# Kernel tuning notes

Hardware: AMD Instinct MI355X
Metric: run time of the kernel (lower is better)

Reference implementation:

```python
import jax, jax.numpy as jnp
import numpy as np

B, N, D = 64, 100, 32            # batch, nodes, node feature size
FE = [96, 160, 192]              # edge-MLP layer sizes
FN = [256, 256, 32]              # node-MLP layer sizes
ALPHA = 0.2                      # leaky relu slope


def _lin_init(key, fan_in, fan_out):
    kw, kb = jax.random.split(key)
    bound = 1.0 / np.sqrt(fan_in)
    w = jax.random.uniform(kw, (fan_in, fan_out), jnp.float32, -bound, bound)
    b = jax.random.uniform(kb, (fan_out,), jnp.float32, -bound, bound)
    return w, b


def setup_inputs() -> dict:
    key = jax.random.key(0)
    ks = jax.random.split(key, 7)
    d = {"x": jax.random.normal(ks[0], (B, N, D), jnp.float32)}
    fe_sizes = [2 * D] + FE                    # edge MLP: in = concat(x_i, x_j)
    fn_sizes = [FE[-1] + D] + FN               # node MLP: in = concat(agg, x)
    for li in range(3):
        w, b = _lin_init(ks[1 + li], fe_sizes[li], fe_sizes[li + 1])
        d[f"fe_w{li}"], d[f"fe_b{li}"] = w, b
    for li in range(3):
        w, b = _lin_init(ks[4 + li], fn_sizes[li], fn_sizes[li + 1])
        d[f"fn_w{li}"], d[f"fn_b{li}"] = w, b
    return d


def reference(x, fe_w0, fe_b0, fe_w1, fe_b1, fe_w2, fe_b2,
              fn_w0, fn_b0, fn_w1, fn_b1, fn_w2, fn_b2):
    b, n, d = x.shape
    lr = lambda v: jax.nn.leaky_relu(v, ALPHA)
    # fully-connected pairwise edge features: A[b,i,j] = concat(x_i, x_j)
    xi = jnp.broadcast_to(x[:, :, None, :], (b, n, n, d))
    xj = jnp.broadcast_to(x[:, None, :, :], (b, n, n, d))
    a = jnp.concatenate([xi, xj], axis=-1)          # [b, n, n, 2d]
    # edge MLP (fe): leaky relu after every layer (final_linear=False)
    a = lr(a @ fe_w0 + fe_b0)
    a = lr(a @ fe_w1 + fe_b1)
    a = lr(a @ fe_w2 + fe_b2)                       # [b, n, n, FE[-1]]
    # sum aggregation over neighbors j
    agg = jnp.sum(a, axis=2)                        # [b, n, FE[-1]]
    # node MLP (fn): final layer linear (final_linear=True)
    h = jnp.concatenate([agg, x], axis=-1)          # [b, n, FE[-1]+d]
    h = lr(h @ fn_w0 + fn_b0)
    h = lr(h @ fn_w1 + fn_b1)
    h = h @ fn_w2 + fn_b2                           # [b, n, FN[-1]]
    return h
```

## Files before the change

### kernel.cpp

```cpp
#include <hip/hip_runtime.h>

#define B_    64
#define N_    100
#define D_    32
#define F0    96
#define F1    160
#define F2    192
#define HID   256
#define FOUT  32

typedef unsigned short u16;
typedef unsigned int   u32;
typedef u16   u16x8 __attribute__((ext_vector_type(8)));
typedef u32   u32x2 __attribute__((ext_vector_type(2)));
typedef __bf16 bf16x8 __attribute__((ext_vector_type(8)));
typedef float  fx4   __attribute__((ext_vector_type(4)));

__device__ __forceinline__ u16 f2bf(float f) {
    return __builtin_bit_cast(u16, (__bf16)f);
}
__device__ __forceinline__ float lrelu(float v) { return fmaxf(v, 0.2f * v); }

__device__ __forceinline__ bf16x8 fragLds(const u16* p) {
    return __builtin_bit_cast(bf16x8, *(const u16x8*)p);
}
__device__ __forceinline__ bf16x8 fragGbl(const u16* __restrict__ p) {
    return __builtin_bit_cast(bf16x8, *(const u16x8*)p);
}
#define MFMA(a, b, c) __builtin_amdgcn_mfma_f32_16x16x32_bf16((a), (b), (c), 0, 0, 0)

__device__ __forceinline__ u32x2 quadPack(u32 h) {
    u32 h1 = (u32)__shfl_xor((int)h, 1, 64);
    u32 pk = h | (h1 << 16);
    u32 pko = (u32)__shfl_xor((int)pk, 2, 64);
    return (u32x2){pk, pko};
}

#define OFF_P     0u
#define OFF_V     2457600u
#define OFF_AGG   4915200u
#define OFF_PACK  7372800u
#define PK_W1     0
#define PK_W2     15360
#define PK_N0     46080
#define PK_N1     103424
#define PK_N2     168960
#define PK_TOTAL  177152

#define PV_BLOCKS 1200
#define PACK_BLOCKS 346

__global__ __launch_bounds__(512) void prep_kernel(
    const float* __restrict__ x,
    const float* __restrict__ few0,
    const float* __restrict__ few1, const float* __restrict__ few2,
    const float* __restrict__ fnw0, const float* __restrict__ fnw1,
    const float* __restrict__ fnw2,
    float* __restrict__ V, u16* __restrict__ wpack)
{
    const int blk = blockIdx.x, tid = threadIdx.x;
    if (blk < PV_BLOCKS) {
        int o = blk * 512 + tid;
        int r = o / F0, k = o - r * F0;
        const float* xr = x + r * D_;
        float acc = 0.f;
        #pragma unroll
        for (int d = 0; d < D_; ++d) acc = fmaf(xr[d], few0[(D_ + d) * F0 + k], acc);
        V[r * F0 + k] = acc;
    } else {
        int p = (blk - PV_BLOCKS) * 512 + tid;
        const float* src; int start, Ncols, NT;
        if (p < PK_W2)      { start = PK_W1; src = few1; Ncols = F1;   NT = 10; }
        else if (p < PK_N0) { start = PK_W2; src = few2; Ncols = F2;   NT = 12; }
        else if (p < PK_N1) { start = PK_N0; src = fnw0; Ncols = HID;  NT = 16; }
        else if (p < PK_N2) { start = PK_N1; src = fnw1; Ncols = HID;  NT = 16; }
        else                { start = PK_N2; src = fnw2; Ncols = FOUT; NT = 2;  }
        int local = p - start;
        int j = local & 7, lane = (local >> 3) & 63, rest = local >> 9;
        int nt = rest % NT, kt = rest / NT;
        int n = 16 * nt + (lane & 15);
        int k = 32 * kt + 8 * (lane >> 4) + j;
        wpack[p] = f2bf(src[k * Ncols + n]);
    }
}

__global__ __launch_bounds__(512, 4) void edge_kernel(
    const float* __restrict__ x, const float* __restrict__ few0,
    const float* __restrict__ feb0, const float* __restrict__ V,
    const u16* __restrict__ W1p, const u16* __restrict__ W2p,
    const float* __restrict__ feb1, const float* __restrict__ feb2,
    u16* __restrict__ agg)
{
    const int i = blockIdx.x, b = blockIdx.y;
    const int tid = threadIdx.x, ld = tid & 63, wv = tid >> 6;
    const int wn = wv & 3, wm = wv >> 2;
    const int row = b * N_ + i;

    __shared__ __align__(16) u16  sA0p[7 * 3 * 512];
    __shared__ __align__(16) u16  sA1p[7 * 5 * 512];
    __shared__ __align__(16) float sP[F0];
    __shared__ __align__(16) float sAggP[2 * F2];

    if (tid < F0) {
        const float* xr = x + (size_t)row * D_;
        float acc = feb0[tid];
        #pragma unroll
        for (int d = 0; d < D_; ++d) acc = fmaf(xr[d], few0[d * F0 + tid], acc);
        sP[tid] = acc;
    }
    __syncthreads();

    {
        const float* Vb = V + (size_t)b * N_ * F0;
        #pragma unroll
        for (int s = 0; s < 3; ++s) {
            int idx = tid + 512 * s;
            if (idx < 1344) {
                int lane = idx & 63, rest = idx >> 6;
                int kt = rest % 3, mt = rest / 3;
                int k = 32 * kt + 8 * (lane >> 4);
                int m = 16 * mt + (lane & 15);
                u16x8 w;
                if (m < N_) {
                    const float* vp = Vb + m * F0 + k;
                    fx4 v0 = *(const fx4*)(vp);
                    fx4 v1 = *(const fx4*)(vp + 4);
                    fx4 p0 = *(const fx4*)(sP + k);
                    fx4 p1 = *(const fx4*)(sP + k + 4);
                    #pragma unroll
                    for (int jj = 0; jj < 4; ++jj) {
                        w[jj]     = f2bf(lrelu(p0[jj] + v0[jj]));
                        w[4 + jj] = f2bf(lrelu(p1[jj] + v1[jj]));
                    }
                } else {
                    w = (u16x8){0, 0, 0, 0, 0, 0, 0, 0};
                }
                *(u16x8*)(sA0p + idx * 8) = w;
            }
        }
    }
    __syncthreads();

    const int mtB = wm ? 4 : 0, mtE = wm ? 7 : 4;
    const int c = ld & 15, rlo = (ld >> 4) * 4;
    const int a1off = (ld * 16) ^ (((ld >> 3) & 7) << 4);

    {
        const int nCnt = (wn < 2) ? 3 : 2;
        bf16x8 bw[3][3]; float bias[3];
        #pragma unroll
        for (int t = 0; t < 3; ++t) if (t < nCnt) {
            int nt = wn + 4 * t;
            bias[t] = feb1[16 * nt + c];
            #pragma unroll
            for (int kt = 0; kt < 3; ++kt)
                bw[t][kt] = fragGbl(W1p + (size_t)((kt * 10 + nt) * 64 + ld) * 8);
        }
        for (int mt = mtB; mt < mtE; ++mt) {
            bf16x8 a[3];
            #pragma unroll
            for (int kt = 0; kt < 3; ++kt)
                a[kt] = fragLds(sA0p + ((mt * 3 + kt) * 64 + ld) * 8);
            fx4 acc[3];
            #pragma unroll
            for (int t = 0; t < 3; ++t) acc[t] = (fx4){0.f, 0.f, 0.f, 0.f};
            #pragma unroll
            for (int kt = 0; kt < 3; ++kt)
                #pragma unroll
                for (int t = 0; t < 3; ++t)
                    if (t < nCnt) acc[t] = MFMA(a[kt], bw[t][kt], acc[t]);
            #pragma unroll
            for (int t = 0; t < 3; ++t) if (t < nCnt) {
                int nt = wn + 4 * t;
                int f = 16 * nt + c;
                int lq = (f >> 3) & 3;
                int S  = (((rlo >> 3) + 2 * lq) & 7) << 4;
                char* base = (char*)sA1p + (mt * 5 + (nt >> 1)) * 1024 + (c & 4) * 2;
                #pragma unroll
                for (int r = 0; r < 4; ++r) {
                    u32 h = (u32)f2bf(lrelu(acc[t][r] + bias[t]));
                    u32x2 two = quadPack(h);
                    int rowl = rlo + 16 * lq + r;
                    if ((ld & 3) == 0)
                        *(u32x2*)(base + ((rowl * 16) ^ S)) = two;
                }
            }
        }
    }
    __syncthreads();

    {
        bf16x8 bw[3][5]; float bias[3];
        float aggp[3] = {0.f, 0.f, 0.f};
        #pragma unroll
        for (int t = 0; t < 3; ++t) {
            int nt = wn + 4 * t;
            bias[t] = feb2[16 * nt + c];
            #pragma unroll
            for (int kt = 0; kt < 5; ++kt)
                bw[t][kt] = fragGbl(W2p + (size_t)((kt * 12 + nt) * 64 + ld) * 8);
        }
        for (int mt = mtB; mt < mtE; ++mt) {
            bf16x8 a[5];
            const char* rb = (const char*)sA1p + mt * 5120 + a1off;
            #pragma unroll
            for (int kt = 0; kt < 5; ++kt)
                a[kt] = fragLds((const u16*)(rb + kt * 1024));
            fx4 acc[3];
            #pragma unroll
            for (int t = 0; t < 3; ++t) acc[t] = (fx4){0.f, 0.f, 0.f, 0.f};
            #pragma unroll
            for (int kt = 0; kt < 5; ++kt)
                #pragma unroll
                for (int t = 0; t < 3; ++t)
                    acc[t] = MFMA(a[kt], bw[t][kt], acc[t]);
            bool ok = (mt < 6) || (rlo == 0);
            if (ok) {
                #pragma unroll
                for (int t = 0; t < 3; ++t)
                    #pragma unroll
                    for (int r = 0; r < 4; ++r)
                        aggp[t] += lrelu(acc[t][r] + bias[t]);
            }
        }
        #pragma unroll
        for (int t = 0; t < 3; ++t) {
            aggp[t] += __shfl_xor(aggp[t], 16, 64);
            aggp[t] += __shfl_xor(aggp[t], 32, 64);
        }
        if (ld < 16) {
            #pragma unroll
            for (int t = 0; t < 3; ++t)
                sAggP[wm * F2 + 16 * (wn + 4 * t) + ld] = aggp[t];
        }
    }
    __syncthreads();

    if (tid < F2) {
        float v = sAggP[tid] + sAggP[F2 + tid];
        agg[(size_t)row * F2 + tid] = f2bf(v);
    }
}

__global__ __launch_bounds__(512, 4) void node_kernel(
    const u16* __restrict__ agg, const float* __restrict__ x,
    const u16* __restrict__ n0p, const u16* __restrict__ n1p,
    const u16* __restrict__ n2p,
    const float* __restrict__ fnb0, const float* __restrict__ fnb1,
    const float* __restrict__ fnb2,
    float* __restrict__ out)
{
    const int blk = blockIdx.x;
    const int tid = threadIdx.x, ld = tid & 63, wv = tid >> 6;
    const int c = ld & 15, rlo = (ld >> 4) * 4;
    const int c0 = c & ~3;

    __shared__ __align__(16) u16 sH0p[7 * 512];
    __shared__ __align__(16) u16 sH1p[8 * 512];
    __shared__ __align__(16) u16 sH2p[8 * 512];

    if (tid < 448) {
        int lane = tid & 63, kt = tid >> 6;
        int k = 32 * kt + 8 * (lane >> 4);
        int m = lane & 15;
        int g = 16 * blk + m;
        u16x8 w;
        if (k < F2) {
            w = *(const u16x8*)(agg + (size_t)g * F2 + k);
        } else {
            const float* xp = x + (size_t)g * D_ + (k - F2);
            fx4 v0 = *(const fx4*)xp;
            fx4 v1 = *(const fx4*)(xp + 4);
            #pragma unroll
            for (int jj = 0; jj < 4; ++jj) {
                w[jj] = f2bf(v0[jj]); w[4 + jj] = f2bf(v1[jj]);
            }
        }
        *(u16x8*)(sH0p + tid * 8) = w;
    }
    __syncthreads();

    {
        fx4 acc[2];
        #pragma unroll
        for (int t = 0; t < 2; ++t) acc[t] = (fx4){0.f, 0.f, 0.f, 0.f};
        for (int kt = 0; kt < 7; ++kt) {
            bf16x8 a = fragLds(sH0p + (kt * 64 + ld) * 8);
            #pragma unroll
            for (int t = 0; t < 2; ++t) {
                int nt = wv + 8 * t;
                bf16x8 bw = fragGbl(n0p + (size_t)((kt * 16 + nt) * 64 + ld) * 8);
                acc[t] = MFMA(a, bw, acc[t]);
            }
        }
        #pragma unroll
        for (int t = 0; t < 2; ++t) {
            int f = 16 * (wv + 8 * t) + c;
            float bias = fnb0[f];
            int kt2 = f >> 5, lq = (f >> 3) & 3;
            u16* basep = sH1p + (kt2 * 64 + rlo + 16 * lq) * 8 + (c0 & 7);
            #pragma unroll
            for (int r = 0; r < 4; ++r) {
                u32 h = (u32)f2bf(lrelu(acc[t][r] + bias));
                u32x2 two = quadPack(h);
                if ((ld & 3) == 0)
                    *(u32x2*)(basep + r * 8) = two;
            }
        }
    }
    __syncthreads();

    {
        fx4 acc[2];
        #pragma unroll
        for (int t = 0; t < 2; ++t) acc[t] = (fx4){0.f, 0.f, 0.f, 0.f};
        for (int kt = 0; kt < 8; ++kt) {
            bf16x8 a = fragLds(sH1p + (kt * 64 + ld) * 8);
            #pragma unroll
            for (int t = 0; t < 2; ++t) {
                int nt = wv + 8 * t;
                bf16x8 bw = fragGbl(n1p + (size_t)((kt * 16 + nt) * 64 + ld) * 8);
                acc[t] = MFMA(a, bw, acc[t]);
            }
        }
        #pragma unroll
        for (int t = 0; t < 2; ++t) {
            int f = 16 * (wv + 8 * t) + c;
            float bias = fnb1[f];
            int kt2 = f >> 5, lq = (f >> 3) & 3;
            u16* basep = sH2p + (kt2 * 64 + rlo + 16 * lq) * 8 + (c0 & 7);
            #pragma unroll
            for (int r = 0; r < 4; ++r) {
                u32 h = (u32)f2bf(lrelu(acc[t][r] + bias));
                u32x2 two = quadPack(h);
                if ((ld & 3) == 0)
                    *(u32x2*)(basep + r * 8) = two;
            }
        }
    }
    __syncthreads();

    if (wv < 2) {
        int nt = wv;
        fx4 acc = (fx4){0.f, 0.f, 0.f, 0.f};
        for (int kt = 0; kt < 8; ++kt) {
            bf16x8 a = fragLds(sH2p + (kt * 64 + ld) * 8);
            bf16x8 bw = fragGbl(n2p + (size_t)((kt * 2 + nt) * 64 + ld) * 8);
            acc = MFMA(a, bw, acc);
        }
        int f = 16 * nt + c;
        float bias = fnb2[f];
        #pragma unroll
        for (int r = 0; r < 4; ++r) {
            int g = 16 * blk + rlo + r;
            out[(size_t)g * FOUT + f] = acc[r] + bias;
        }
    }
}

extern "C" void kernel_launch(void* const* d_in, const int* in_sizes, int n_in,
                              void* d_out, int out_size, void* d_ws, size_t ws_size,
                              hipStream_t stream) {
    const float* x    = (const float*)d_in[0];
    const float* few0 = (const float*)d_in[1];
    const float* feb0 = (const float*)d_in[2];
    const float* few1 = (const float*)d_in[3];
    const float* feb1 = (const float*)d_in[4];
    const float* few2 = (const float*)d_in[5];
    const float* feb2 = (const float*)d_in[6];
    const float* fnw0 = (const float*)d_in[7];
    const float* fnb0 = (const float*)d_in[8];
    const float* fnw1 = (const float*)d_in[9];
    const float* fnb1 = (const float*)d_in[10];
    const float* fnw2 = (const float*)d_in[11];
    const float* fnb2 = (const float*)d_in[12];

    char* w = (char*)d_ws;
    float* V    = (float*)(w + OFF_V);
    u16*   aggb = (u16*)(w + OFF_AGG);
    u16*   pack = (u16*)(w + OFF_PACK);

    prep_kernel<<<PV_BLOCKS + PACK_BLOCKS, 512, 0, stream>>>(
        x, few0, few1, few2, fnw0, fnw1, fnw2, V, pack);

    edge_kernel<<<dim3(N_, B_), 512, 0, stream>>>(
        x, few0, feb0, V, pack + PK_W1, pack + PK_W2, feb1, feb2, aggb);

    node_kernel<<<400, 512, 0, stream>>>(
        aggb, x, pack + PK_N0, pack + PK_N1, pack + PK_N2,
        fnb0, fnb1, fnb2, (float*)d_out);
}
```

Before: 239.1 us.

## Assign one M-tile per wave in edge MLP, fusing layers without barrier

```diff
diff --git a/kernel.cpp b/kernel.cpp
--- a/kernel.cpp
+++ b/kernel.cpp
@@ -93,13 +93,12 @@
 {
     const int i = blockIdx.x, b = blockIdx.y;
     const int tid = threadIdx.x, ld = tid & 63, wv = tid >> 6;
-    const int wn = wv & 3, wm = wv >> 2;
     const int row = b * N_ + i;
 
     __shared__ __align__(16) u16  sA0p[7 * 3 * 512];
     __shared__ __align__(16) u16  sA1p[7 * 5 * 512];
     __shared__ __align__(16) float sP[F0];
-    __shared__ __align__(16) float sAggP[2 * F2];
+    __shared__ __align__(16) float sAggP[7 * F2];
 
     if (tid < F0) {
         const float* xr = x + (size_t)row * D_;
@@ -141,37 +140,39 @@
     }
     __syncthreads();
 
-    const int mtB = wm ? 4 : 0, mtE = wm ? 7 : 4;
     const int c = ld & 15, rlo = (ld >> 4) * 4;
     const int a1off = (ld * 16) ^ (((ld >> 3) & 7) << 4);
 
-    {
-        const int nCnt = (wn < 2) ? 3 : 2;
-        bf16x8 bw[3][3]; float bias[3];
-        #pragma unroll
-        for (int t = 0; t < 3; ++t) if (t < nCnt) {
-            int nt = wn + 4 * t;
-            bias[t] = feb1[16 * nt + c];
+    if (wv < 7) {
+        const int mt = wv;
+
+        bf16x8 a0[3];
+        #pragma unroll
+        for (int kt = 0; kt < 3; ++kt)
+            a0[kt] = fragLds(sA0p + ((mt * 3 + kt) * 64 + ld) * 8);
+        #pragma unroll
+        for (int g = 0; g < 4; ++g) {
+            const int cnt = (g < 3) ? 3 : 1;
+            bf16x8 bw[3][3]; float bias[3];
+            #pragma unroll
+            for (int t = 0; t < 3; ++t) if (t < cnt) {
+                int nt = 3 * g + t;
+                bias[t] = feb1[16 * nt + c];
+                #pragma unroll
+                for (int kt = 0; kt < 3; ++kt)
+                    bw[t][kt] = fragGbl(W1p + (size_t)((kt * 10 + nt) * 64 + ld) * 8);
+            }
+            fx4 acc[3];
+            #pragma unroll
+            for (int t = 0; t < 3; ++t) acc[t] = (fx4){0.f, 0.f, 0.f, 0.f};
             #pragma unroll
             for (int kt = 0; kt < 3; ++kt)
-                bw[t][kt] = fragGbl(W1p + (size_t)((kt * 10 + nt) * 64 + ld) * 8);
-        }
-        for (int mt = mtB; mt < mtE; ++mt) {
-            bf16x8 a[3];
-            #pragma unroll
-            for (int kt = 0; kt < 3; ++kt)
-                a[kt] = fragLds(sA0p + ((mt * 3 + kt) * 64 + ld) * 8);
-            fx4 acc[3];
-            #pragma unroll
-            for (int t = 0; t < 3; ++t) acc[t] = (fx4){0.f, 0.f, 0.f, 0.f};
-            #pragma unroll
-            for (int kt = 0; kt < 3; ++kt)
                 #pragma unroll
                 for (int t = 0; t < 3; ++t)
-                    if (t < nCnt) acc[t] = MFMA(a[kt], bw[t][kt], acc[t]);
-            #pragma unroll
-            for (int t = 0; t < 3; ++t) if (t < nCnt) {
-                int nt = wn + 4 * t;
+                    if (t < cnt) acc[t] = MFMA(a0[kt], bw[t][kt], acc[t]);
+            #pragma unroll
+            for (int t = 0; t < 3; ++t) if (t < cnt) {
+                int nt = 3 * g + t;
                 int f = 16 * nt + c;
                 int lq = (f >> 3) & 3;
                 int S  = (((rlo >> 3) + 2 * lq) & 7) << 4;
@@ -186,58 +187,59 @@
                 }
             }
         }
-    }
-    __syncthreads();
-
-    {
-        bf16x8 bw[3][5]; float bias[3];
-        float aggp[3] = {0.f, 0.f, 0.f};
-        #pragma unroll
-        for (int t = 0; t < 3; ++t) {
-            int nt = wn + 4 * t;
-            bias[t] = feb2[16 * nt + c];
+
+        bf16x8 a1[5];
+        {
+            const char* rb = (const char*)sA1p + mt * 5120 + a1off;
             #pragma unroll
             for (int kt = 0; kt < 5; ++kt)
-                bw[t][kt] = fragGbl(W2p + (size_t)((kt * 12 + nt) * 64 + ld) * 8);
-        }
-        for (int mt = mtB; mt < mtE; ++mt) {
-            bf16x8 a[5];
-            const char* rb = (const char*)sA1p + mt * 5120 + a1off;
+                a1[kt] = fragLds((const u16*)(rb + kt * 1024));
+        }
+        #pragma unroll
+        for (int g = 0; g < 4; ++g) {
+            bf16x8 bw[3][5]; float bias[3];
+            #pragma unroll
+            for (int t = 0; t < 3; ++t) {
+                int nt = 3 * g + t;
+                bias[t] = feb2[16 * nt + c];
+                #pragma unroll
+                for (int kt = 0; kt < 5; ++kt)
+                    bw[t][kt] = fragGbl(W2p + (size_t)((kt * 12 + nt) * 64 + ld) * 8);
+            }
+            fx4 acc[3];
+            #pragma unroll
+            for (int t = 0; t < 3; ++t) acc[t] = (fx4){0.f, 0.f, 0.f, 0.f};
             #pragma unroll
             for (int kt = 0; kt < 5; ++kt)
-                a[kt] = fragLds((const u16*)(rb + kt * 1024));
-            fx4 acc[3];
-            #pragma unroll
-            for (int t = 0; t < 3; ++t) acc[t] = (fx4){0.f, 0.f, 0.f, 0.f};
-            #pragma unroll
-            for (int kt = 0; kt < 5; ++kt)
                 #pragma unroll
                 for (int t = 0; t < 3; ++t)
-                    acc[t] = MFMA(a[kt], bw[t][kt], acc[t]);
-            bool ok = (mt < 6) || (rlo == 0);
-            if (ok) {
-                #pragma unroll
-                for (int t = 0; t < 3; ++t)
+                    acc[t] = MFMA(a1[kt], bw[t][kt], acc[t]);
+            float aggp[3];
+            #pragma unroll
+            for (int t = 0; t < 3; ++t) {
+                float s = 0.f;
+                if ((mt < 6) || (rlo == 0)) {
                     #pragma unroll
                     for (int r = 0; r < 4; ++r)
-                        aggp[t] += lrelu(acc[t][r] + bias[t]);
-            }
-        }
-        #pragma unroll
-        for (int t = 0; t < 3; ++t) {
-            aggp[t] += __shfl_xor(aggp[t], 16, 64);
-            aggp[t] += __shfl_xor(aggp[t], 32, 64);
-        }
-        if (ld < 16) {
-            #pragma unroll
-            for (int t = 0; t < 3; ++t)
-                sAggP[wm * F2 + 16 * (wn + 4 * t) + ld] = aggp[t];
+                        s += lrelu(acc[t][r] + bias[t]);
+                }
+                s += __shfl_xor(s, 16, 64);
+                s += __shfl_xor(s, 32, 64);
+                aggp[t] = s;
+            }
+            if (ld < 16) {
+                #pragma unroll
+                for (int t = 0; t < 3; ++t)
+                    sAggP[wv * F2 + 16 * (3 * g + t) + ld] = aggp[t];
+            }
         }
     }
     __syncthreads();
 
     if (tid < F2) {
-        float v = sAggP[tid] + sAggP[F2 + tid];
+        float v = sAggP[tid];
+        #pragma unroll
+        for (int w = 1; w < 7; ++w) v += sAggP[w * F2 + tid];
         agg[(size_t)row * F2 + tid] = f2bf(v);
     }
 }
```

Result: slower. 278.4 us (+16.5%).
